# Kernel optimization log

Hardware: AMD Instinct MI355X
Metric: run time of the kernel (lower is better)

The kernel has to match this reference:

```python
import jax, jax.numpy as jnp
import numpy as np
from math import sqrt

B, H, S, D = 4, 16, 8192, 64
M = 64  # num_samples (<= D since ortho_features=True)
SCALE = 0.1  # keep exp() numerically sane for randn inputs


def _gram_schmidt(mat):
    # unnormalized Gram-Schmidt over columns, matching the torch module
    d, m = mat.shape
    out = np.zeros_like(mat)
    out[:, 0] = mat[:, 0]
    for i in range(1, m):
        v = mat[:, i]
        U = out[:, :i]                      # [d, i]
        coef = (U.T @ v) / np.sum(U * U, axis=0)
        out[:, i] = v - U @ coef
    return out


def setup_inputs() -> dict:
    key = jax.random.key(0)
    kq, kk, kv = jax.random.split(key, 3)
    query = jax.random.normal(kq, (B, H, S, D), dtype=jnp.float32) * SCALE
    key_t = jax.random.normal(kk, (B, H, S, D), dtype=jnp.float32) * SCALE
    value = jax.random.normal(kv, (B, H, S, D), dtype=jnp.float32) * SCALE
    rng = np.random.default_rng(0)
    omega = jnp.asarray(_gram_schmidt(rng.standard_normal((D, M)).astype(np.float32)))
    return {"query": query, "key": key_t, "value": value, "omega": omega}


def _pos_features(x, omega, m):
    # 1/sqrt(m) * exp(-||x||^2/2) * exp(x @ omega)   -> [..., S, m]
    h = jnp.exp(-0.5 * jnp.sum(x * x, axis=-1)) * (1.0 / sqrt(m))  # [B,H,S]
    return h[..., None] * jnp.exp(jnp.einsum('bhsd,dm->bhsm', x, omega))


def reference(query, key, value, omega):
    d = query.shape[-1]
    m = omega.shape[-1]
    q_prime = _pos_features(query, omega, m)   # [B,H,S,m]
    k_prime = _pos_features(key, omega, m)     # [B,H,S,m]
    ones = jnp.ones(value.shape[:-1] + (1,), dtype=value.dtype)
    C = jnp.concatenate([value, ones], axis=-1)               # [B,H,S,d+1]
    buf1 = jnp.einsum('bhsm,bhsc->bhmc', k_prime, C)          # [B,H,m,d+1]
    buf2 = jnp.einsum('bhsm,bhmc->bhsc', q_prime, buf1)       # [B,H,S,d+1]
    num = buf2[..., :d]                                       # [B,H,S,d]
    den = buf2[..., d:]                                       # [B,H,S,1]
    return num / den
```

## Files before the change

kernel.cpp:

```cpp
#include <hip/hip_runtime.h>

typedef short short8 __attribute__((ext_vector_type(8)));
typedef float f32x4 __attribute__((ext_vector_type(4)));

namespace {
constexpr int Sc = 8192, Dc = 64;
constexpr int NH = 64;
constexpr int CH = 512;
constexpr int TPT = CH / 64;
constexpr int NCHUNK = Sc / CH;
constexpr size_t DEN_OFF = (size_t)NH * 4096;
constexpr size_t WT_OFF_BYTES = (DEN_OFF + NH * 64) * 4;
}

__device__ __forceinline__ void bsplit(float x, short& hi, short& lo) {
  unsigned u = __builtin_bit_cast(unsigned, x);
  unsigned rh = (u + 0x7fffu + ((u >> 16) & 1u)) & 0xffff0000u;
  hi = (short)(rh >> 16);
  float res = x - __builtin_bit_cast(float, rh);
  lo = (short)(__builtin_bit_cast(unsigned, res) >> 16);
}
__device__ __forceinline__ unsigned pk2(short lo16, short hi16) {
  return (unsigned)(unsigned short)lo16 | ((unsigned)(unsigned short)hi16 << 16);
}

__global__ void p0(const float* __restrict__ omega, short* __restrict__ wT) {
  int i = blockIdx.x * 256 + threadIdx.x;
  if (i < 4096) {
    int m = i >> 6, d = i & 63;
    short hi, lo;
    bsplit(omega[d * 64 + m], hi, lo);
    wT[m * 64 + d] = hi;
    wT[4096 + m * 64 + d] = lo;
  }
}

__global__ __launch_bounds__(256, 2) void p1(
    const float* __restrict__ Kg, const float* __restrict__ Vg,
    const short* __restrict__ wT, float* __restrict__ b1, float* __restrict__ den) {
  __shared__ short Kh[64 * 72], Kl[64 * 72];
  __shared__ unsigned VT[64 * 64];
  __shared__ short PTh[64 * 72], PTl[64 * 72];
  __shared__ float ssq[64];

  const int t = threadIdx.x;
  const int lane = t & 63;
  const int w = t >> 6;
  const int a = lane & 15;
  const int g = lane >> 4;
  const int bh = blockIdx.x / NCHUNK, ch = blockIdx.x % NCHUNK;
  const float* Kb = Kg + ((size_t)bh * Sc + (size_t)ch * CH) * Dc;
  const float* Vb = Vg + ((size_t)bh * Sc + (size_t)ch * CH) * Dc;

  short8 wfh[4][2], wfl[4][2];
#pragma unroll
  for (int mt = 0; mt < 4; ++mt)
#pragma unroll
    for (int ks = 0; ks < 2; ++ks) {
      int off = (a + 16 * mt) * 64 + 32 * ks + 8 * g;
      wfh[mt][ks] = *(const short8*)(wT + off);
      wfl[mt][ks] = *(const short8*)(wT + 4096 + off);
    }

  float4 kreg[4], vreg[4];
  auto load_tile = [&](int tile) {
    const float4* Kt = (const float4*)(Kb + (size_t)tile * 64 * Dc);
    const float4* Vt = (const float4*)(Vb + (size_t)tile * 64 * Dc);
#pragma unroll
    for (int rr = 0; rr < 4; ++rr) {
      kreg[rr] = Kt[rr * 256 + t];
      vreg[rr] = Vt[rr * 256 + t];
    }
  };
  auto store_tile = [&]() {
#pragma unroll
    for (int rr = 0; rr < 4; ++rr) {
      int idx = rr * 256 + t;
      int row = idx >> 4;
      int c4 = idx & 15;
      float4 kv = kreg[rr];
      short h0, h1, h2, h3, l0, l1, l2, l3;
      bsplit(kv.x, h0, l0); bsplit(kv.y, h1, l1);
      bsplit(kv.z, h2, l2); bsplit(kv.w, h3, l3);
      uint2 uh, ul;
      uh.x = pk2(h0, h1); uh.y = pk2(h2, h3);
      ul.x = pk2(l0, l1); ul.y = pk2(l2, l3);
      *(uint2*)&Kh[row * 72 + c4 * 4] = uh;
      *(uint2*)&Kl[row * 72 + c4 * 4] = ul;
      float ps = kv.x * kv.x + kv.y * kv.y + kv.z * kv.z + kv.w * kv.w;
      ps += __shfl_xor(ps, 1, 64); ps += __shfl_xor(ps, 2, 64);
      ps += __shfl_xor(ps, 4, 64); ps += __shfl_xor(ps, 8, 64);
      if (c4 == 0) ssq[row] = ps;
      float4 vv = vreg[rr];
      int swz = 8 * (c4 & 7);
      short vh_, vl_;
      bsplit(vv.x, vh_, vl_); VT[(4 * c4 + 0) * 64 + (row ^ swz)] = pk2(vh_, vl_);
      bsplit(vv.y, vh_, vl_); VT[(4 * c4 + 1) * 64 + (row ^ swz)] = pk2(vh_, vl_);
      bsplit(vv.z, vh_, vl_); VT[(4 * c4 + 2) * 64 + (row ^ swz)] = pk2(vh_, vl_);
      bsplit(vv.w, vh_, vl_); VT[(4 * c4 + 3) * 64 + (row ^ swz)] = pk2(vh_, vl_);
    }
  };

  f32x4 B1a[4];
#pragma unroll
  for (int ct = 0; ct < 4; ++ct) B1a[ct] = (f32x4){0.f, 0.f, 0.f, 0.f};
  float dpart[4] = {0.f, 0.f, 0.f, 0.f};

  load_tile(0);
  store_tile();
  __syncthreads();

  for (int tile = 0; tile < TPT; ++tile) {
    if (tile + 1 < TPT) load_tile(tile + 1);

    f32x4 X[4];
#pragma unroll
    for (int mt = 0; mt < 4; ++mt) X[mt] = (f32x4){0.f, 0.f, 0.f, 0.f};
#pragma unroll
    for (int ks = 0; ks < 2; ++ks) {
      short8 ah = *(const short8*)&Kh[(16 * w + a) * 72 + 32 * ks + 8 * g];
      short8 al = *(const short8*)&Kl[(16 * w + a) * 72 + 32 * ks + 8 * g];
#pragma unroll
      for (int mt = 0; mt < 4; ++mt) {
        X[mt] = __builtin_amdgcn_mfma_f32_16x16x32_bf16(ah, wfh[mt][ks], X[mt], 0, 0, 0);
        X[mt] = __builtin_amdgcn_mfma_f32_16x16x32_bf16(ah, wfl[mt][ks], X[mt], 0, 0, 0);
        X[mt] = __builtin_amdgcn_mfma_f32_16x16x32_bf16(al, wfh[mt][ks], X[mt], 0, 0, 0);
      }
    }

    float sq[4];
#pragma unroll
    for (int r = 0; r < 4; ++r) sq[r] = ssq[16 * w + 4 * g + r];
#pragma unroll
    for (int mt = 0; mt < 4; ++mt) {
      short ph[4], pl[4];
#pragma unroll
      for (int r = 0; r < 4; ++r) {
        float p = 0.125f * __expf(X[mt][r] - 0.5f * sq[r]);
        dpart[mt] += p;
        bsplit(p, ph[r], pl[r]);
      }
      uint2 uh, ul;
      uh.x = pk2(ph[0], ph[1]); uh.y = pk2(ph[2], ph[3]);
      ul.x = pk2(pl[0], pl[1]); ul.y = pk2(pl[2], pl[3]);
      *(uint2*)&PTh[(16 * mt + a) * 72 + 16 * w + 4 * g] = uh;
      *(uint2*)&PTl[(16 * mt + a) * 72 + 16 * w + 4 * g] = ul;
    }
    __syncthreads();

#pragma unroll
    for (int ks = 0; ks < 2; ++ks) {
      short8 pah = *(const short8*)&PTh[(16 * w + a) * 72 + 32 * ks + 8 * g];
      short8 pal = *(const short8*)&PTl[(16 * w + a) * 72 + 32 * ks + 8 * g];
#pragma unroll
      for (int ct = 0; ct < 4; ++ct) {
        int c = 16 * ct + a;
        int s0 = (32 * ks + 8 * g) ^ (8 * ((c >> 2) & 7));
        const unsigned* vp = &VT[c * 64 + s0];
        uint4 q0 = *(const uint4*)vp;
        uint4 q1 = *(const uint4*)(vp + 4);
        short8 vh, vl;
        vh[0] = (short)(q0.x & 0xffff); vl[0] = (short)(q0.x >> 16);
        vh[1] = (short)(q0.y & 0xffff); vl[1] = (short)(q0.y >> 16);
        vh[2] = (short)(q0.z & 0xffff); vl[2] = (short)(q0.z >> 16);
        vh[3] = (short)(q0.w & 0xffff); vl[3] = (short)(q0.w >> 16);
        vh[4] = (short)(q1.x & 0xffff); vl[4] = (short)(q1.x >> 16);
        vh[5] = (short)(q1.y & 0xffff); vl[5] = (short)(q1.y >> 16);
        vh[6] = (short)(q1.z & 0xffff); vl[6] = (short)(q1.z >> 16);
        vh[7] = (short)(q1.w & 0xffff); vl[7] = (short)(q1.w >> 16);
        B1a[ct] = __builtin_amdgcn_mfma_f32_16x16x32_bf16(pah, vh, B1a[ct], 0, 0, 0);
        B1a[ct] = __builtin_amdgcn_mfma_f32_16x16x32_bf16(pah, vl, B1a[ct], 0, 0, 0);
        B1a[ct] = __builtin_amdgcn_mfma_f32_16x16x32_bf16(pal, vh, B1a[ct], 0, 0, 0);
      }
    }
    __syncthreads();
    if (tile + 1 < TPT) store_tile();
    __syncthreads();
  }

  float* b1h = b1 + (size_t)bh * 4096;
#pragma unroll
  for (int ct = 0; ct < 4; ++ct)
#pragma unroll
    for (int r = 0; r < 4; ++r)
      atomicAdd(&b1h[(16 * w + 4 * g + r) * 64 + 16 * ct + a], B1a[ct][r]);
#pragma unroll
  for (int mt = 0; mt < 4; ++mt) {
    float v = dpart[mt];
    v += __shfl_xor(v, 16, 64);
    v += __shfl_xor(v, 32, 64);
    if (g == 0) atomicAdd(&den[bh * 64 + 16 * mt + a], v);
  }
}

__global__ __launch_bounds__(256, 2) void p2(
    const float* __restrict__ Qg, const short* __restrict__ wT,
    const float* __restrict__ b1, const float* __restrict__ den,
    float* __restrict__ out) {
  __shared__ short Qh[64 * 72], Ql[64 * 72];
  __shared__ unsigned QP[64 * 68];
  __shared__ short B1h[64 * 72], B1l[64 * 72];
  __shared__ float denv[64];
  __shared__ float ssq[64];

  const int t = threadIdx.x;
  const int lane = t & 63;
  const int w = t >> 6;
  const int a = lane & 15;
  const int g = lane >> 4;
  const int bh = blockIdx.x / NCHUNK, ch = blockIdx.x % NCHUNK;
  const float* Qb = Qg + ((size_t)bh * Sc + (size_t)ch * CH) * Dc;

  short8 wfh[4][2], wfl[4][2];
#pragma unroll
  for (int mt = 0; mt < 4; ++mt)
#pragma unroll
    for (int ks = 0; ks < 2; ++ks) {
      int off = (a + 16 * mt) * 64 + 32 * ks + 8 * g;
      wfh[mt][ks] = *(const short8*)(wT + off);
      wfl[mt][ks] = *(const short8*)(wT + 4096 + off);
    }

  const float* b1g = b1 + (size_t)bh * 4096;
  for (int i = t; i < 4096; i += 256) {
    int m = i >> 6, c = i & 63;
    short hi, lo;
    bsplit(b1g[i], hi, lo);
    B1h[c * 72 + m] = hi;
    B1l[c * 72 + m] = lo;
  }
  if (t < 64) denv[t] = den[bh * 64 + t];

  float4 qreg[4];
  auto load_tile = [&](int tile) {
    const float4* Qt = (const float4*)(Qb + (size_t)tile * 64 * Dc);
#pragma unroll
    for (int rr = 0; rr < 4; ++rr) qreg[rr] = Qt[rr * 256 + t];
  };
  auto store_tile = [&]() {
#pragma unroll
    for (int rr = 0; rr < 4; ++rr) {
      int idx = rr * 256 + t;
      int row = idx >> 4;
      int c4 = idx & 15;
      float4 kv = qreg[rr];
      short h0, h1, h2, h3, l0, l1, l2, l3;
      bsplit(kv.x, h0, l0); bsplit(kv.y, h1, l1);
      bsplit(kv.z, h2, l2); bsplit(kv.w, h3, l3);
      uint2 uh, ul;
      uh.x = pk2(h0, h1); uh.y = pk2(h2, h3);
      ul.x = pk2(l0, l1); ul.y = pk2(l2, l3);
      *(uint2*)&Qh[row * 72 + c4 * 4] = uh;
      *(uint2*)&Ql[row * 72 + c4 * 4] = ul;
      float ps = kv.x * kv.x + kv.y * kv.y + kv.z * kv.z + kv.w * kv.w;
      ps += __shfl_xor(ps, 1, 64); ps += __shfl_xor(ps, 2, 64);
      ps += __shfl_xor(ps, 4, 64); ps += __shfl_xor(ps, 8, 64);
      if (c4 == 0) ssq[row] = ps;
    }
  };

  load_tile(0);
  store_tile();
  __syncthreads();

  for (int tile = 0; tile < TPT; ++tile) {
    if (tile + 1 < TPT) load_tile(tile + 1);

    f32x4 X[4];
#pragma unroll
    for (int mt = 0; mt < 4; ++mt) X[mt] = (f32x4){0.f, 0.f, 0.f, 0.f};
#pragma unroll
    for (int ks = 0; ks < 2; ++ks) {
      short8 ah = *(const short8*)&Qh[(16 * w + a) * 72 + 32 * ks + 8 * g];
      short8 al = *(const short8*)&Ql[(16 * w + a) * 72 + 32 * ks + 8 * g];
#pragma unroll
      for (int mt = 0; mt < 4; ++mt) {
        X[mt] = __builtin_amdgcn_mfma_f32_16x16x32_bf16(ah, wfh[mt][ks], X[mt], 0, 0, 0);
        X[mt] = __builtin_amdgcn_mfma_f32_16x16x32_bf16(ah, wfl[mt][ks], X[mt], 0, 0, 0);
        X[mt] = __builtin_amdgcn_mfma_f32_16x16x32_bf16(al, wfh[mt][ks], X[mt], 0, 0, 0);
      }
    }

    float sq[4];
#pragma unroll
    for (int r = 0; r < 4; ++r) sq[r] = ssq[16 * w + 4 * g + r];
    float dv[4];
#pragma unroll
    for (int mt = 0; mt < 4; ++mt) dv[mt] = denv[16 * mt + a];
    float dn[4] = {0.f, 0.f, 0.f, 0.f};
#pragma unroll
    for (int mt = 0; mt < 4; ++mt) {
#pragma unroll
      for (int r = 0; r < 4; ++r) {
        float p = 0.125f * __expf(X[mt][r] - 0.5f * sq[r]);
        dn[r] = fmaf(p, dv[mt], dn[r]);
        short hi, lo;
        bsplit(p, hi, lo);
        QP[(16 * w + 4 * g + r) * 68 + 16 * mt + a] = pk2(hi, lo);
      }
    }
#pragma unroll
    for (int r = 0; r < 4; ++r) {
      dn[r] += __shfl_xor(dn[r], 1, 64);
      dn[r] += __shfl_xor(dn[r], 2, 64);
      dn[r] += __shfl_xor(dn[r], 4, 64);
      dn[r] += __shfl_xor(dn[r], 8, 64);
    }
    __syncthreads();

    f32x4 O[4];
#pragma unroll
    for (int ct = 0; ct < 4; ++ct) O[ct] = (f32x4){0.f, 0.f, 0.f, 0.f};
#pragma unroll
    for (int ks = 0; ks < 2; ++ks) {
      const unsigned* qp = &QP[(16 * w + a) * 68 + 32 * ks + 8 * g];
      uint4 q0 = *(const uint4*)qp;
      uint4 q1 = *(const uint4*)(qp + 4);
      short8 qh, ql;
      qh[0] = (short)(q0.x & 0xffff); ql[0] = (short)(q0.x >> 16);
      qh[1] = (short)(q0.y & 0xffff); ql[1] = (short)(q0.y >> 16);
      qh[2] = (short)(q0.z & 0xffff); ql[2] = (short)(q0.z >> 16);
      qh[3] = (short)(q0.w & 0xffff); ql[3] = (short)(q0.w >> 16);
      qh[4] = (short)(q1.x & 0xffff); ql[4] = (short)(q1.x >> 16);
      qh[5] = (short)(q1.y & 0xffff); ql[5] = (short)(q1.y >> 16);
      qh[6] = (short)(q1.z & 0xffff); ql[6] = (short)(q1.z >> 16);
      qh[7] = (short)(q1.w & 0xffff); ql[7] = (short)(q1.w >> 16);
#pragma unroll
      for (int ct = 0; ct < 4; ++ct) {
        short8 bh_ = *(const short8*)&B1h[(16 * ct + a) * 72 + 32 * ks + 8 * g];
        short8 bl_ = *(const short8*)&B1l[(16 * ct + a) * 72 + 32 * ks + 8 * g];
        O[ct] = __builtin_amdgcn_mfma_f32_16x16x32_bf16(qh, bh_, O[ct], 0, 0, 0);
        O[ct] = __builtin_amdgcn_mfma_f32_16x16x32_bf16(qh, bl_, O[ct], 0, 0, 0);
        O[ct] = __builtin_amdgcn_mfma_f32_16x16x32_bf16(ql, bh_, O[ct], 0, 0, 0);
      }
    }

    float inv[4];
#pragma unroll
    for (int r = 0; r < 4; ++r) inv[r] = 1.0f / dn[r];
    float* ob = out + ((size_t)bh * Sc + (size_t)ch * CH + tile * 64 + 16 * w + 4 * g) * 64;
#pragma unroll
    for (int ct = 0; ct < 4; ++ct)
#pragma unroll
      for (int r = 0; r < 4; ++r)
        ob[r * 64 + 16 * ct + a] = O[ct][r] * inv[r];
    __syncthreads();
    if (tile + 1 < TPT) store_tile();
    __syncthreads();
  }
}

extern "C" void kernel_launch(void* const* d_in, const int* in_sizes, int n_in,
                              void* d_out, int out_size, void* d_ws, size_t ws_size,
                              hipStream_t stream) {
  const float* Q = (const float*)d_in[0];
  const float* K = (const float*)d_in[1];
  const float* V = (const float*)d_in[2];
  const float* omega = (const float*)d_in[3];
  float* outp = (float*)d_out;
  float* b1 = (float*)d_ws;
  float* den = b1 + DEN_OFF;
  short* wT = (short*)((char*)d_ws + WT_OFF_BYTES);

  hipMemsetAsync(d_ws, 0, WT_OFF_BYTES, stream);
  p0<<<16, 256, 0, stream>>>(omega, wT);
  p1<<<NH * NCHUNK, 256, 0, stream>>>(K, V, wT, b1, den);
  p2<<<NH * NCHUNK, 256, 0, stream>>>(Q, wT, b1, den, outp);
}
```

Measured before the change: 167.2 us.

## Pack bf16 hi/lo pairs into single LDS words and double chunk size

Replaces the separate hi and lo bf16 LDS arrays for K, Q and P with one interleaved 32-bit word per element, padded to a row stride of 68. The hi and lo MFMA operands are then pulled out with v_perm instead of per-element shifts. The V transpose swizzle is reworked for the new stride, and the per-block sequence chunk grows from 512 to 1024 rows. This is meant to cut LDS store instructions and unpack ALU work, and to halve the number of atomic partial-sum flushes, at the cost of fewer blocks and so less parallelism.

```diff
diff --git a/kernel.cpp b/kernel.cpp
--- a/kernel.cpp
+++ b/kernel.cpp
@@ -6,22 +6,39 @@
 namespace {
 constexpr int Sc = 8192, Dc = 64;
 constexpr int NH = 64;
-constexpr int CH = 512;
+constexpr int CH = 1024;
 constexpr int TPT = CH / 64;
 constexpr int NCHUNK = Sc / CH;
 constexpr size_t DEN_OFF = (size_t)NH * 4096;
 constexpr size_t WT_OFF_BYTES = (DEN_OFF + NH * 64) * 4;
 }
 
-__device__ __forceinline__ void bsplit(float x, short& hi, short& lo) {
+__device__ __forceinline__ unsigned pkhl(float x) {
   unsigned u = __builtin_bit_cast(unsigned, x);
   unsigned rh = (u + 0x7fffu + ((u >> 16) & 1u)) & 0xffff0000u;
-  hi = (short)(rh >> 16);
   float res = x - __builtin_bit_cast(float, rh);
-  lo = (short)(__builtin_bit_cast(unsigned, res) >> 16);
-}
-__device__ __forceinline__ unsigned pk2(short lo16, short hi16) {
-  return (unsigned)(unsigned short)lo16 | ((unsigned)(unsigned short)hi16 << 16);
+  return (rh >> 16) | (__builtin_bit_cast(unsigned, res) & 0xffff0000u);
+}
+__device__ __forceinline__ void bsplit(float x, short& hi, short& lo) {
+  unsigned p = pkhl(x);
+  hi = (short)(p & 0xffff);
+  lo = (short)(p >> 16);
+}
+__device__ __forceinline__ short8 exhi(uint4 q0, uint4 q1) {
+  union { unsigned u[4]; short8 s; } r;
+  r.u[0] = __builtin_amdgcn_perm(q0.y, q0.x, 0x05040100u);
+  r.u[1] = __builtin_amdgcn_perm(q0.w, q0.z, 0x05040100u);
+  r.u[2] = __builtin_amdgcn_perm(q1.y, q1.x, 0x05040100u);
+  r.u[3] = __builtin_amdgcn_perm(q1.w, q1.z, 0x05040100u);
+  return r.s;
+}
+__device__ __forceinline__ short8 exlo(uint4 q0, uint4 q1) {
+  union { unsigned u[4]; short8 s; } r;
+  r.u[0] = __builtin_amdgcn_perm(q0.y, q0.x, 0x07060302u);
+  r.u[1] = __builtin_amdgcn_perm(q0.w, q0.z, 0x07060302u);
+  r.u[2] = __builtin_amdgcn_perm(q1.y, q1.x, 0x07060302u);
+  r.u[3] = __builtin_amdgcn_perm(q1.w, q1.z, 0x07060302u);
+  return r.s;
 }
 
 __global__ void p0(const float* __restrict__ omega, short* __restrict__ wT) {
@@ -38,9 +55,9 @@
 __global__ __launch_bounds__(256, 2) void p1(
     const float* __restrict__ Kg, const float* __restrict__ Vg,
     const short* __restrict__ wT, float* __restrict__ b1, float* __restrict__ den) {
-  __shared__ short Kh[64 * 72], Kl[64 * 72];
-  __shared__ unsigned VT[64 * 64];
-  __shared__ short PTh[64 * 72], PTl[64 * 72];
+  __shared__ unsigned Kpk[64 * 68];
+  __shared__ unsigned VT[64 * 68];
+  __shared__ unsigned PT[64 * 68];
   __shared__ float ssq[64];
 
   const int t = threadIdx.x;
@@ -79,25 +96,20 @@
       int row = idx >> 4;
       int c4 = idx & 15;
       float4 kv = kreg[rr];
-      short h0, h1, h2, h3, l0, l1, l2, l3;
-      bsplit(kv.x, h0, l0); bsplit(kv.y, h1, l1);
-      bsplit(kv.z, h2, l2); bsplit(kv.w, h3, l3);
-      uint2 uh, ul;
-      uh.x = pk2(h0, h1); uh.y = pk2(h2, h3);
-      ul.x = pk2(l0, l1); ul.y = pk2(l2, l3);
-      *(uint2*)&Kh[row * 72 + c4 * 4] = uh;
-      *(uint2*)&Kl[row * 72 + c4 * 4] = ul;
+      uint4 kp;
+      kp.x = pkhl(kv.x); kp.y = pkhl(kv.y);
+      kp.z = pkhl(kv.z); kp.w = pkhl(kv.w);
+      *(uint4*)&Kpk[row * 68 + 4 * c4] = kp;
       float ps = kv.x * kv.x + kv.y * kv.y + kv.z * kv.z + kv.w * kv.w;
       ps += __shfl_xor(ps, 1, 64); ps += __shfl_xor(ps, 2, 64);
       ps += __shfl_xor(ps, 4, 64); ps += __shfl_xor(ps, 8, 64);
       if (c4 == 0) ssq[row] = ps;
       float4 vv = vreg[rr];
-      int swz = 8 * (c4 & 7);
-      short vh_, vl_;
-      bsplit(vv.x, vh_, vl_); VT[(4 * c4 + 0) * 64 + (row ^ swz)] = pk2(vh_, vl_);
-      bsplit(vv.y, vh_, vl_); VT[(4 * c4 + 1) * 64 + (row ^ swz)] = pk2(vh_, vl_);
-      bsplit(vv.z, vh_, vl_); VT[(4 * c4 + 2) * 64 + (row ^ swz)] = pk2(vh_, vl_);
-      bsplit(vv.w, vh_, vl_); VT[(4 * c4 + 3) * 64 + (row ^ swz)] = pk2(vh_, vl_);
+      int sw = row ^ (4 * ((c4 >> 1) & 7));
+      VT[(4 * c4 + 0) * 68 + sw] = pkhl(vv.x);
+      VT[(4 * c4 + 1) * 68 + sw] = pkhl(vv.y);
+      VT[(4 * c4 + 2) * 68 + sw] = pkhl(vv.z);
+      VT[(4 * c4 + 3) * 68 + sw] = pkhl(vv.w);
     }
   };
 
@@ -118,8 +130,10 @@
     for (int mt = 0; mt < 4; ++mt) X[mt] = (f32x4){0.f, 0.f, 0.f, 0.f};
 #pragma unroll
     for (int ks = 0; ks < 2; ++ks) {
-      short8 ah = *(const short8*)&Kh[(16 * w + a) * 72 + 32 * ks + 8 * g];
-      short8 al = *(const short8*)&Kl[(16 * w + a) * 72 + 32 * ks + 8 * g];
+      const unsigned* kb = &Kpk[(16 * w + a) * 68 + 32 * ks + 8 * g];
+      uint4 q0 = *(const uint4*)kb;
+      uint4 q1 = *(const uint4*)(kb + 4);
+      short8 ah = exhi(q0, q1), al = exlo(q0, q1);
 #pragma unroll
       for (int mt = 0; mt < 4; ++mt) {
         X[mt] = __builtin_amdgcn_mfma_f32_16x16x32_bf16(ah, wfh[mt][ks], X[mt], 0, 0, 0);
@@ -133,41 +147,32 @@
     for (int r = 0; r < 4; ++r) sq[r] = ssq[16 * w + 4 * g + r];
 #pragma unroll
     for (int mt = 0; mt < 4; ++mt) {
-      short ph[4], pl[4];
-#pragma unroll
-      for (int r = 0; r < 4; ++r) {
-        float p = 0.125f * __expf(X[mt][r] - 0.5f * sq[r]);
-        dpart[mt] += p;
-        bsplit(p, ph[r], pl[r]);
-      }
-      uint2 uh, ul;
-      uh.x = pk2(ph[0], ph[1]); uh.y = pk2(ph[2], ph[3]);
-      ul.x = pk2(pl[0], pl[1]); ul.y = pk2(pl[2], pl[3]);
-      *(uint2*)&PTh[(16 * mt + a) * 72 + 16 * w + 4 * g] = uh;
-      *(uint2*)&PTl[(16 * mt + a) * 72 + 16 * w + 4 * g] = ul;
-    }
-    __syncthreads();
-
-#pragma unroll
-    for (int ks = 0; ks < 2; ++ks) {
-      short8 pah = *(const short8*)&PTh[(16 * w + a) * 72 + 32 * ks + 8 * g];
-      short8 pal = *(const short8*)&PTl[(16 * w + a) * 72 + 32 * ks + 8 * g];
+      uint4 pp;
+      float p_;
+      p_ = 0.125f * __expf(X[mt][0] - 0.5f * sq[0]); dpart[mt] += p_; pp.x = pkhl(p_);
+      p_ = 0.125f * __expf(X[mt][1] - 0.5f * sq[1]); dpart[mt] += p_; pp.y = pkhl(p_);
+      p_ = 0.125f * __expf(X[mt][2] - 0.5f * sq[2]); dpart[mt] += p_; pp.z = pkhl(p_);
+      p_ = 0.125f * __expf(X[mt][3] - 0.5f * sq[3]); dpart[mt] += p_; pp.w = pkhl(p_);
+      *(uint4*)&PT[(16 * mt + a) * 68 + 16 * w + 4 * g] = pp;
+    }
+    __syncthreads();
+
+#pragma unroll
+    for (int ks = 0; ks < 2; ++ks) {
+      const unsigned* pb = &PT[(16 * w + a) * 68 + 32 * ks + 8 * g];
+      uint4 r0 = *(const uint4*)pb;
+      uint4 r1 = *(const uint4*)(pb + 4);
+      short8 pah = exhi(r0, r1), pal = exlo(r0, r1);
 #pragma unroll
       for (int ct = 0; ct < 4; ++ct) {
         int c = 16 * ct + a;
-        int s0 = (32 * ks + 8 * g) ^ (8 * ((c >> 2) & 7));
-        const unsigned* vp = &VT[c * 64 + s0];
-        uint4 q0 = *(const uint4*)vp;
-        uint4 q1 = *(const uint4*)(vp + 4);
-        short8 vh, vl;
-        vh[0] = (short)(q0.x & 0xffff); vl[0] = (short)(q0.x >> 16);
-        vh[1] = (short)(q0.y & 0xffff); vl[1] = (short)(q0.y >> 16);
-        vh[2] = (short)(q0.z & 0xffff); vl[2] = (short)(q0.z >> 16);
-        vh[3] = (short)(q0.w & 0xffff); vl[3] = (short)(q0.w >> 16);
-        vh[4] = (short)(q1.x & 0xffff); vl[4] = (short)(q1.x >> 16);
-        vh[5] = (short)(q1.y & 0xffff); vl[5] = (short)(q1.y >> 16);
-        vh[6] = (short)(q1.z & 0xffff); vl[6] = (short)(q1.z >> 16);
-        vh[7] = (short)(q1.w & 0xffff); vl[7] = (short)(q1.w >> 16);
+        int kk4 = 4 * ((2 * ct + (a >> 3)) & 7);
+        int s0 = (32 * ks + 8 * g) ^ kk4;
+        int s1 = (32 * ks + 8 * g + 4) ^ kk4;
+        const unsigned* vb = &VT[c * 68];
+        uint4 v0 = *(const uint4*)(vb + s0);
+        uint4 v1 = *(const uint4*)(vb + s1);
+        short8 vh = exhi(v0, v1), vl = exlo(v0, v1);
         B1a[ct] = __builtin_amdgcn_mfma_f32_16x16x32_bf16(pah, vh, B1a[ct], 0, 0, 0);
         B1a[ct] = __builtin_amdgcn_mfma_f32_16x16x32_bf16(pah, vl, B1a[ct], 0, 0, 0);
         B1a[ct] = __builtin_amdgcn_mfma_f32_16x16x32_bf16(pal, vh, B1a[ct], 0, 0, 0);
@@ -197,7 +202,7 @@
     const float* __restrict__ Qg, const short* __restrict__ wT,
     const float* __restrict__ b1, const float* __restrict__ den,
     float* __restrict__ out) {
-  __shared__ short Qh[64 * 72], Ql[64 * 72];
+  __shared__ unsigned Qpk[64 * 68];
   __shared__ unsigned QP[64 * 68];
   __shared__ short B1h[64 * 72], B1l[64 * 72];
   __shared__ float denv[64];
@@ -244,14 +249,10 @@
       int row = idx >> 4;
       int c4 = idx & 15;
       float4 kv = qreg[rr];
-      short h0, h1, h2, h3, l0, l1, l2, l3;
-      bsplit(kv.x, h0, l0); bsplit(kv.y, h1, l1);
-      bsplit(kv.z, h2, l2); bsplit(kv.w, h3, l3);
-      uint2 uh, ul;
-      uh.x = pk2(h0, h1); uh.y = pk2(h2, h3);
-      ul.x = pk2(l0, l1); ul.y = pk2(l2, l3);
-      *(uint2*)&Qh[row * 72 + c4 * 4] = uh;
-      *(uint2*)&Ql[row * 72 + c4 * 4] = ul;
+      uint4 qp;
+      qp.x = pkhl(kv.x); qp.y = pkhl(kv.y);
+      qp.z = pkhl(kv.z); qp.w = pkhl(kv.w);
+      *(uint4*)&Qpk[row * 68 + 4 * c4] = qp;
       float ps = kv.x * kv.x + kv.y * kv.y + kv.z * kv.z + kv.w * kv.w;
       ps += __shfl_xor(ps, 1, 64); ps += __shfl_xor(ps, 2, 64);
       ps += __shfl_xor(ps, 4, 64); ps += __shfl_xor(ps, 8, 64);
@@ -271,8 +272,10 @@
     for (int mt = 0; mt < 4; ++mt) X[mt] = (f32x4){0.f, 0.f, 0.f, 0.f};
 #pragma unroll
     for (int ks = 0; ks < 2; ++ks) {
-      short8 ah = *(const short8*)&Qh[(16 * w + a) * 72 + 32 * ks + 8 * g];
-      short8 al = *(const short8*)&Ql[(16 * w + a) * 72 + 32 * ks + 8 * g];
+      const unsigned* qb = &Qpk[(16 * w + a) * 68 + 32 * ks + 8 * g];
+      uint4 q0 = *(const uint4*)qb;
+      uint4 q1 = *(const uint4*)(qb + 4);
+      short8 ah = exhi(q0, q1), al = exlo(q0, q1);
 #pragma unroll
       for (int mt = 0; mt < 4; ++mt) {
         X[mt] = __builtin_amdgcn_mfma_f32_16x16x32_bf16(ah, wfh[mt][ks], X[mt], 0, 0, 0);
@@ -292,11 +295,9 @@
     for (int mt = 0; mt < 4; ++mt) {
 #pragma unroll
       for (int r = 0; r < 4; ++r) {
-        float p = 0.125f * __expf(X[mt][r] - 0.5f * sq[r]);
-        dn[r] = fmaf(p, dv[mt], dn[r]);
-        short hi, lo;
-        bsplit(p, hi, lo);
-        QP[(16 * w + 4 * g + r) * 68 + 16 * mt + a] = pk2(hi, lo);
+        float p_ = 0.125f * __expf(X[mt][r] - 0.5f * sq[r]);
+        dn[r] = fmaf(p_, dv[mt], dn[r]);
+        QP[(16 * w + 4 * g + r) * 68 + 16 * mt + a] = pkhl(p_);
       }
     }
 #pragma unroll
@@ -313,18 +314,10 @@
     for (int ct = 0; ct < 4; ++ct) O[ct] = (f32x4){0.f, 0.f, 0.f, 0.f};
 #pragma unroll
     for (int ks = 0; ks < 2; ++ks) {
-      const unsigned* qp = &QP[(16 * w + a) * 68 + 32 * ks + 8 * g];
-      uint4 q0 = *(const uint4*)qp;
-      uint4 q1 = *(const uint4*)(qp + 4);
-      short8 qh, ql;
-      qh[0] = (short)(q0.x & 0xffff); ql[0] = (short)(q0.x >> 16);
-      qh[1] = (short)(q0.y & 0xffff); ql[1] = (short)(q0.y >> 16);
-      qh[2] = (short)(q0.z & 0xffff); ql[2] = (short)(q0.z >> 16);
-      qh[3] = (short)(q0.w & 0xffff); ql[3] = (short)(q0.w >> 16);
-      qh[4] = (short)(q1.x & 0xffff); ql[4] = (short)(q1.x >> 16);
-      qh[5] = (short)(q1.y & 0xffff); ql[5] = (short)(q1.y >> 16);
-      qh[6] = (short)(q1.z & 0xffff); ql[6] = (short)(q1.z >> 16);
-      qh[7] = (short)(q1.w & 0xffff); ql[7] = (short)(q1.w >> 16);
+      const unsigned* qb = &QP[(16 * w + a) * 68 + 32 * ks + 8 * g];
+      uint4 r0 = *(const uint4*)qb;
+      uint4 r1 = *(const uint4*)(qb + 4);
+      short8 qh = exhi(r0, r1), ql = exlo(r0, r1);
 #pragma unroll
       for (int ct = 0; ct < 4; ++ct) {
         short8 bh_ = *(const short8*)&B1h[(16 * ct + a) * 72 + 32 * ks + 8 * g];
```

After: 146.6 us. 1.14x faster.
